# Optimization experiments

Hardware: AMD Instinct MI355X
Metric: run time of the kernel (lower is better)

## Reference

```python
import jax, jax.numpy as jnp
import numpy as np

BETA = 1.0  # inverse temperature (default of retrieve())
EPS = 1e-12  # matches torch F.normalize eps


def _l2_normalize(x):
    # torch.nn.functional.normalize(p=2, dim=-1): x / max(||x||, eps)
    n = jnp.sqrt(jnp.sum(x * x, axis=-1, keepdims=True))
    return x / jnp.maximum(n, EPS)


def setup_inputs() -> dict:
    key = jax.random.key(0)
    kq, kk = jax.random.split(key)
    N, K, D = 65536, 4096, 128
    queries = jax.random.normal(kq, (N, D), dtype=jnp.float32)
    # learnable memory keys, init_std = 0.02
    keys = jax.random.normal(kk, (K, D), dtype=jnp.float32) * 0.02
    return {"queries": queries, "keys": keys}


def reference(queries, keys):
    # normalize_keys=True, normalize_queries=True
    k_n = _l2_normalize(keys)
    q_n = _l2_normalize(queries)
    # values are TIED to the raw keys parameter (get_values returns self.keys,
    # un-normalized) — only the score-side keys are normalized.
    values = keys
    scores = BETA * jnp.einsum('nd,kd->nk', q_n, k_n)  # [N, K]
    attention = jax.nn.softmax(scores, axis=-1)
    retrieved = jnp.einsum('nk,kd->nd', attention, values)  # [N, D]
    return retrieved
```

## Files before the change

### kernel.cpp

```cpp
#include <hip/hip_runtime.h>
#include <hip/hip_bf16.h>
#include <stdint.h>


typedef __attribute__((ext_vector_type(8))) short bf16x8;
typedef __attribute__((ext_vector_type(16))) float f32x16;

#define MFMA32(a, b, c) __builtin_amdgcn_mfma_f32_32x32x16_bf16(a, b, c, 0, 0, 0)

__device__ __forceinline__ unsigned pkbf(float lo, float hi) {
  union { __hip_bfloat162 h2; unsigned u; } v;
  v.h2 = __float22bfloat162_rn(float2{lo, hi});
  return v.u;
}

__global__ __launch_bounds__(256) void prep_k(const float* __restrict__ k,
                                              char* __restrict__ knf,
                                              char* __restrict__ vtf, int K) {
  __shared__ float sRaw[64 * 132];
  __shared__ float sScale[64];
  const int tid = threadIdx.x;
  const int kbase = blockIdx.x * 64;
  {
    const int key_loc = tid >> 2, dq = tid & 3;
    const float4* src = (const float4*)(k + (size_t)(kbase + key_loc) * 128 + dq * 32);
    float4 f[8];
    float ss = 0.f;
#pragma unroll
    for (int i = 0; i < 8; ++i) {
      f[i] = src[i];
      ss += f[i].x * f[i].x + f[i].y * f[i].y + f[i].z * f[i].z + f[i].w * f[i].w;
    }
    ss += __shfl_xor(ss, 1);
    ss += __shfl_xor(ss, 2);
    float4* dst = (float4*)(sRaw + key_loc * 132 + dq * 32);
#pragma unroll
    for (int i = 0; i < 8; ++i) dst[i] = f[i];
    if (dq == 0) sScale[key_loc] = ss > 0.f ? rsqrtf(ss) : 0.f;
  }
  __syncthreads();

#pragma unroll
  for (int r = 0; r < 4; ++r) {
    const int c = r * 256 + tid;
    const int t_loc = c >> 9, ds = (c >> 6) & 7, l = c & 63;
    const int h5 = l >> 5, c32 = l & 31;
    const int key_loc = t_loc * 32 + c32;
    const float sc = sScale[key_loc];
    const float* p = sRaw + key_loc * 132 + ds * 16 + h5 * 8;
    uint4 w;
    w.x = pkbf(p[0] * sc, p[1] * sc);
    w.y = pkbf(p[2] * sc, p[3] * sc);
    w.z = pkbf(p[4] * sc, p[5] * sc);
    w.w = pkbf(p[6] * sc, p[7] * sc);
    *(uint4*)(knf + ((size_t)blockIdx.x * 1024 + c) * 16) = w;
  }
#pragma unroll
  for (int r = 0; r < 4; ++r) {
    const int c = r * 256 + tid;
    const int s = c >> 8, db2 = (c >> 6) & 3, l = c & 63;
    const int h5 = l >> 5, c32 = l & 31;
    const int d = db2 * 32 + c32;
    const int kb = (s >> 1) * 32 + (s & 1) * 8 + h5 * 4;
    float f[8];
#pragma unroll
    for (int j = 0; j < 8; ++j)
      f[j] = sRaw[(kb + (j & 3) + (j >> 2) * 16) * 132 + d];
    uint4 w;
    w.x = pkbf(f[0], f[1]);
    w.y = pkbf(f[2], f[3]);
    w.z = pkbf(f[4], f[5]);
    w.w = pkbf(f[6], f[7]);
    *(uint4*)(vtf + ((size_t)blockIdx.x * 1024 + c) * 16) = w;
  }
}

__global__ __launch_bounds__(256) void attn_main(
    const float* __restrict__ q, const char* __restrict__ knf,
    const char* __restrict__ vtf, float* __restrict__ out, int K) {
  __shared__ __align__(16) char sE[16384];
  const int tid = threadIdx.x;
  const int wave = tid >> 6, lane = tid & 63;
  const int h5 = lane >> 5, c32 = lane & 31;
  const int qrow0 = blockIdx.x * 128 + wave * 32;

  bf16x8 qf[8];
  {
    const float* qr = q + (size_t)(qrow0 + c32) * 128;
    float f[64];
    float ss = 0.f;
#pragma unroll
    for (int ds = 0; ds < 8; ++ds) {
      const float4 a = *(const float4*)(qr + ds * 16 + h5 * 8);
      const float4 b = *(const float4*)(qr + ds * 16 + h5 * 8 + 4);
      f[ds * 8 + 0] = a.x; f[ds * 8 + 1] = a.y; f[ds * 8 + 2] = a.z; f[ds * 8 + 3] = a.w;
      f[ds * 8 + 4] = b.x; f[ds * 8 + 5] = b.y; f[ds * 8 + 6] = b.z; f[ds * 8 + 7] = b.w;
    }
#pragma unroll
    for (int i = 0; i < 64; ++i) ss += f[i] * f[i];
    ss += __shfl_xor(ss, 32);
    const float sc = (ss > 0.f ? rsqrtf(ss) : 0.f) * 1.44269504f;
#pragma unroll
    for (int ds = 0; ds < 8; ++ds) {
      union { unsigned u[4]; bf16x8 v; } t;
#pragma unroll
      for (int p = 0; p < 4; ++p)
        t.u[p] = pkbf(f[ds * 8 + 2 * p] * sc, f[ds * 8 + 2 * p + 1] * sc);
      qf[ds] = t.v;
    }
  }

  f32x16 acc[4];
#pragma unroll
  for (int db2 = 0; db2 < 4; ++db2)
#pragma unroll
    for (int r = 0; r < 16; ++r) acc[db2][r] = 0.f;
  float den = 0.f;
  f32x16 Zf;
#pragma unroll
  for (int r = 0; r < 16; ++r) Zf[r] = 0.f;

  const int nIter = K >> 5;

  auto body = [&](int it, bf16x8 (&kfC)[8], bf16x8 (&kfN)[8]) {
    const int itn = (it + 1 < nIter) ? it + 1 : it;
#pragma unroll
    for (int ds = 0; ds < 8; ++ds)
      kfN[ds] = *(const bf16x8*)(knf + (size_t)itn * 8192 + ds * 1024 + lane * 16);
    bf16x8 vf[8];
#pragma unroll
    for (int j = 0; j < 8; ++j)
      vf[j] = *(const bf16x8*)(vtf + (size_t)it * 8192 + j * 1024 + lane * 16);
    f32x16 S;
#pragma unroll
    for (int ds = 0; ds < 8; ++ds)
      S = MFMA32(kfC[ds], qf[ds], (ds == 0) ? Zf : S);
#pragma unroll
    for (int w = 0; w < 2; ++w) {
      float e[8];
#pragma unroll
      for (int j = 0; j < 8; ++j) {
        const int rr = w * 4 + (j & 3) + (j >> 2) * 8;
        e[j] = __builtin_amdgcn_exp2f(S[rr]);
      }
      den += ((e[0] + e[1]) + (e[2] + e[3])) + ((e[4] + e[5]) + (e[6] + e[7]));
      union { unsigned u[4]; bf16x8 v; } pf;
#pragma unroll
      for (int j2 = 0; j2 < 4; ++j2) pf.u[j2] = pkbf(e[2 * j2], e[2 * j2 + 1]);
#pragma unroll
      for (int db2 = 0; db2 < 4; ++db2)
        acc[db2] = MFMA32(vf[w * 4 + db2], pf.v, acc[db2]);
    }
  };

  bf16x8 kfA[8], kfB[8];
#pragma unroll
  for (int ds = 0; ds < 8; ++ds)
    kfA[ds] = *(const bf16x8*)(knf + ds * 1024 + lane * 16);
  for (int it = 0; it < nIter; it += 2) {
    body(it, kfA, kfB);
    body(it + 1, kfB, kfA);
  }

  den += __shfl_xor(den, 32);
  const float rd = 1.0f / den;

  float* wls = (float*)(sE + wave * 4096);
#pragma unroll
  for (int db2 = 0; db2 < 4; ++db2) {
#pragma unroll
    for (int qd = 0; qd < 4; ++qd) {
      float4 v;
      v.x = acc[db2][qd * 4 + 0] * rd;
      v.y = acc[db2][qd * 4 + 1] * rd;
      v.z = acc[db2][qd * 4 + 2] * rd;
      v.w = acc[db2][qd * 4 + 3] * rd;
      *(float4*)(wls + c32 * 32 + (((h5 + 2 * qd) ^ (c32 & 7)) << 2)) = v;
    }
#pragma unroll
    for (int p = 0; p < 4; ++p) {
      const int ql = p * 8 + (lane >> 3);
      const int x = lane & 7;
      const float4 v = *(const float4*)(wls + ql * 32 + ((x ^ (ql & 7)) << 2));
      *(float4*)(out + (size_t)(qrow0 + ql) * 128 + db2 * 32 + x * 4) = v;
    }
  }
}

extern "C" void kernel_launch(void* const* d_in, const int* in_sizes, int n_in,
                              void* d_out, int out_size, void* d_ws, size_t ws_size,
                              hipStream_t stream) {
  const float* q = (const float*)d_in[0];
  const float* k = (const float*)d_in[1];
  const int N = in_sizes[0] / 128;
  const int K = in_sizes[1] / 128;
  char* ws = (char*)d_ws;
  char* knf = ws;
  char* vtf = ws + (size_t)K * 256;
  float* out = (float*)d_out;

  prep_k<<<dim3(K / 64), dim3(256), 0, stream>>>(k, knf, vtf, K);
  attn_main<<<dim3(N / 128), dim3(256), 0, stream>>>(q, knf, vtf, out, K);
}
```

Before: 225.3 us.

## Split value dimension across grid and process two query tiles per wave

Result: slower. 285.4 us (+26.7%).

```diff
diff --git a/kernel.cpp b/kernel.cpp
--- a/kernel.cpp
+++ b/kernel.cpp
@@ -75,18 +75,20 @@
   }
 }
 
-__global__ __launch_bounds__(256) void attn_main(
+__global__ __launch_bounds__(256, 2) void attn_main(
     const float* __restrict__ q, const char* __restrict__ knf,
     const char* __restrict__ vtf, float* __restrict__ out, int K) {
   __shared__ __align__(16) char sE[16384];
   const int tid = threadIdx.x;
   const int wave = tid >> 6, lane = tid & 63;
   const int h5 = lane >> 5, c32 = lane & 31;
-  const int qrow0 = blockIdx.x * 128 + wave * 32;
-
-  bf16x8 qf[8];
-  {
-    const float* qr = q + (size_t)(qrow0 + c32) * 128;
+  const int split = blockIdx.y;
+  const int qrow0 = blockIdx.x * 256 + wave * 64;
+
+  bf16x8 qf[2][8];
+#pragma unroll
+  for (int qt = 0; qt < 2; ++qt) {
+    const float* qr = q + (size_t)(qrow0 + qt * 32 + c32) * 128;
     float f[64];
     float ss = 0.f;
 #pragma unroll
@@ -106,85 +108,101 @@
 #pragma unroll
       for (int p = 0; p < 4; ++p)
         t.u[p] = pkbf(f[ds * 8 + 2 * p] * sc, f[ds * 8 + 2 * p + 1] * sc);
-      qf[ds] = t.v;
-    }
-  }
-
-  f32x16 acc[4];
-#pragma unroll
-  for (int db2 = 0; db2 < 4; ++db2)
-#pragma unroll
-    for (int r = 0; r < 16; ++r) acc[db2][r] = 0.f;
-  float den = 0.f;
+      qf[qt][ds] = t.v;
+    }
+  }
+
+  f32x16 acc[2][2];
+#pragma unroll
+  for (int dt = 0; dt < 2; ++dt)
+#pragma unroll
+    for (int qt = 0; qt < 2; ++qt)
+#pragma unroll
+      for (int r = 0; r < 16; ++r) acc[dt][qt][r] = 0.f;
+  float den[2] = {0.f, 0.f};
   f32x16 Zf;
 #pragma unroll
   for (int r = 0; r < 16; ++r) Zf[r] = 0.f;
 
   const int nIter = K >> 5;
-
-  auto body = [&](int it, bf16x8 (&kfC)[8], bf16x8 (&kfN)[8]) {
-    const int itn = (it + 1 < nIter) ? it + 1 : it;
+  const char* vsp = vtf + split * 2048;
+
+#pragma unroll 2
+  for (int it = 0; it < nIter; ++it) {
+    bf16x8 kf[8];
 #pragma unroll
     for (int ds = 0; ds < 8; ++ds)
-      kfN[ds] = *(const bf16x8*)(knf + (size_t)itn * 8192 + ds * 1024 + lane * 16);
-    bf16x8 vf[8];
-#pragma unroll
-    for (int j = 0; j < 8; ++j)
-      vf[j] = *(const bf16x8*)(vtf + (size_t)it * 8192 + j * 1024 + lane * 16);
-    f32x16 S;
-#pragma unroll
-    for (int ds = 0; ds < 8; ++ds)
-      S = MFMA32(kfC[ds], qf[ds], (ds == 0) ? Zf : S);
+      kf[ds] = *(const bf16x8*)(knf + (size_t)it * 8192 + ds * 1024 + lane * 16);
+    bf16x8 vf[2][2];
+#pragma unroll
+    for (int w = 0; w < 2; ++w)
+#pragma unroll
+      for (int dt = 0; dt < 2; ++dt)
+        vf[w][dt] = *(const bf16x8*)(vsp + (size_t)(it * 2 + w) * 4096 +
+                                     dt * 1024 + lane * 16);
+
+    f32x16 S[2];
+#pragma unroll
+    for (int qt = 0; qt < 2; ++qt) {
+      f32x16 s;
+#pragma unroll
+      for (int ds = 0; ds < 8; ++ds)
+        s = MFMA32(kf[ds], qf[qt][ds], (ds == 0) ? Zf : s);
+      S[qt] = s;
+    }
+
 #pragma unroll
     for (int w = 0; w < 2; ++w) {
-      float e[8];
-#pragma unroll
-      for (int j = 0; j < 8; ++j) {
-        const int rr = w * 4 + (j & 3) + (j >> 2) * 8;
-        e[j] = __builtin_amdgcn_exp2f(S[rr]);
+#pragma unroll
+      for (int qt = 0; qt < 2; ++qt) {
+        float e[8];
+#pragma unroll
+        for (int j = 0; j < 8; ++j) {
+          const int rr = w * 4 + (j & 3) + (j >> 2) * 8;
+          e[j] = __builtin_amdgcn_exp2f(S[qt][rr]);
+        }
+        den[qt] += ((e[0] + e[1]) + (e[2] + e[3])) + ((e[4] + e[5]) + (e[6] + e[7]));
+        union { unsigned u[4]; bf16x8 v; } pf;
+#pragma unroll
+        for (int j2 = 0; j2 < 4; ++j2) pf.u[j2] = pkbf(e[2 * j2], e[2 * j2 + 1]);
+#pragma unroll
+        for (int dt = 0; dt < 2; ++dt)
+          acc[dt][qt] = MFMA32(vf[w][dt], pf.v, acc[dt][qt]);
       }
-      den += ((e[0] + e[1]) + (e[2] + e[3])) + ((e[4] + e[5]) + (e[6] + e[7]));
-      union { unsigned u[4]; bf16x8 v; } pf;
-#pragma unroll
-      for (int j2 = 0; j2 < 4; ++j2) pf.u[j2] = pkbf(e[2 * j2], e[2 * j2 + 1]);
-#pragma unroll
-      for (int db2 = 0; db2 < 4; ++db2)
-        acc[db2] = MFMA32(vf[w * 4 + db2], pf.v, acc[db2]);
-    }
-  };
-
-  bf16x8 kfA[8], kfB[8];
-#pragma unroll
-  for (int ds = 0; ds < 8; ++ds)
-    kfA[ds] = *(const bf16x8*)(knf + ds * 1024 + lane * 16);
-  for (int it = 0; it < nIter; it += 2) {
-    body(it, kfA, kfB);
-    body(it + 1, kfB, kfA);
-  }
-
-  den += __shfl_xor(den, 32);
-  const float rd = 1.0f / den;
+    }
+  }
+
+  float rd[2];
+#pragma unroll
+  for (int qt = 0; qt < 2; ++qt) {
+    float d = den[qt];
+    d += __shfl_xor(d, 32);
+    rd[qt] = 1.0f / d;
+  }
 
   float* wls = (float*)(sE + wave * 4096);
 #pragma unroll
-  for (int db2 = 0; db2 < 4; ++db2) {
-#pragma unroll
-    for (int qd = 0; qd < 4; ++qd) {
-      float4 v;
-      v.x = acc[db2][qd * 4 + 0] * rd;
-      v.y = acc[db2][qd * 4 + 1] * rd;
-      v.z = acc[db2][qd * 4 + 2] * rd;
-      v.w = acc[db2][qd * 4 + 3] * rd;
-      *(float4*)(wls + c32 * 32 + (((h5 + 2 * qd) ^ (c32 & 7)) << 2)) = v;
-    }
-#pragma unroll
-    for (int p = 0; p < 4; ++p) {
-      const int ql = p * 8 + (lane >> 3);
-      const int x = lane & 7;
-      const float4 v = *(const float4*)(wls + ql * 32 + ((x ^ (ql & 7)) << 2));
-      *(float4*)(out + (size_t)(qrow0 + ql) * 128 + db2 * 32 + x * 4) = v;
-    }
-  }
+  for (int dt = 0; dt < 2; ++dt)
+#pragma unroll
+    for (int qt = 0; qt < 2; ++qt) {
+#pragma unroll
+      for (int qd = 0; qd < 4; ++qd) {
+        float4 v;
+        v.x = acc[dt][qt][qd * 4 + 0] * rd[qt];
+        v.y = acc[dt][qt][qd * 4 + 1] * rd[qt];
+        v.z = acc[dt][qt][qd * 4 + 2] * rd[qt];
+        v.w = acc[dt][qt][qd * 4 + 3] * rd[qt];
+        *(float4*)(wls + c32 * 32 + (((h5 + 2 * qd) ^ (c32 & 7)) << 2)) = v;
+      }
+#pragma unroll
+      for (int p = 0; p < 4; ++p) {
+        const int ql = p * 8 + (lane >> 3);
+        const int x = lane & 7;
+        const float4 v = *(const float4*)(wls + ql * 32 + ((x ^ (ql & 7)) << 2));
+        *(float4*)(out + (size_t)(qrow0 + qt * 32 + ql) * 128 + split * 64 +
+                   dt * 32 + x * 4) = v;
+      }
+    }
 }
 
 extern "C" void kernel_launch(void* const* d_in, const int* in_sizes, int n_in,
@@ -200,5 +218,5 @@
   float* out = (float*)d_out;
 
   prep_k<<<dim3(K / 64), dim3(256), 0, stream>>>(k, knf, vtf, K);
-  attn_main<<<dim3(N / 128), dim3(256), 0, stream>>>(q, knf, vtf, out, K);
-}
+  attn_main<<<dim3(N / 256, 2), dim3(256), 0, stream>>>(q, knf, vtf, out, K);
+}
```

## Split QK MFMA chain and alternate software-pipeline schedules across blocks

Applied to the files above, without the earlier changes.

Result: slower. 272.5 us (+21.0%).

```diff
diff --git a/kernel.cpp b/kernel.cpp
--- a/kernel.cpp
+++ b/kernel.cpp
@@ -122,26 +122,31 @@
 
   const int nIter = K >> 5;
 
-  auto body = [&](int it, bf16x8 (&kfC)[8], bf16x8 (&kfN)[8]) {
-    const int itn = (it + 1 < nIter) ? it + 1 : it;
+  auto loadK = [&](int it, bf16x8 (&kf)[8]) {
+    if (it >= nIter) it = nIter - 1;
 #pragma unroll
     for (int ds = 0; ds < 8; ++ds)
-      kfN[ds] = *(const bf16x8*)(knf + (size_t)itn * 8192 + ds * 1024 + lane * 16);
-    bf16x8 vf[8];
+      kf[ds] = *(const bf16x8*)(knf + (size_t)it * 8192 + ds * 1024 + lane * 16);
+  };
+  auto loadV = [&](int it, bf16x8 (&vf)[8]) {
 #pragma unroll
     for (int j = 0; j < 8; ++j)
       vf[j] = *(const bf16x8*)(vtf + (size_t)it * 8192 + j * 1024 + lane * 16);
-    f32x16 S;
-#pragma unroll
-    for (int ds = 0; ds < 8; ++ds)
-      S = MFMA32(kfC[ds], qf[ds], (ds == 0) ? Zf : S);
+  };
+  auto computeS = [&](const bf16x8 (&kf)[8], f32x16& s0, f32x16& s1) {
+#pragma unroll
+    for (int ds = 0; ds < 4; ++ds) s0 = MFMA32(kf[ds], qf[ds], ds ? s0 : Zf);
+#pragma unroll
+    for (int ds = 4; ds < 8; ++ds) s1 = MFMA32(kf[ds], qf[ds], ds > 4 ? s1 : Zf);
+  };
+  auto expPV = [&](const bf16x8 (&vf)[8], const f32x16& s0, const f32x16& s1) {
 #pragma unroll
     for (int w = 0; w < 2; ++w) {
       float e[8];
 #pragma unroll
       for (int j = 0; j < 8; ++j) {
         const int rr = w * 4 + (j & 3) + (j >> 2) * 8;
-        e[j] = __builtin_amdgcn_exp2f(S[rr]);
+        e[j] = __builtin_amdgcn_exp2f(s0[rr] + s1[rr]);
       }
       den += ((e[0] + e[1]) + (e[2] + e[3])) + ((e[4] + e[5]) + (e[6] + e[7]));
       union { unsigned u[4]; bf16x8 v; } pf;
@@ -153,13 +158,33 @@
     }
   };
 
-  bf16x8 kfA[8], kfB[8];
-#pragma unroll
-  for (int ds = 0; ds < 8; ++ds)
-    kfA[ds] = *(const bf16x8*)(knf + ds * 1024 + lane * 16);
-  for (int it = 0; it < nIter; it += 2) {
-    body(it, kfA, kfB);
-    body(it + 1, kfB, kfA);
+  const int rot = (blockIdx.x ^ (blockIdx.x >> 3) ^ (blockIdx.x >> 8)) & 1;
+
+  bf16x8 kfA[8], kfB[8], vfS[8];
+  f32x16 s0, s1;
+  if (!rot) {
+    loadK(0, kfA);
+    for (int it = 0; it < nIter; it += 2) {
+      loadK(it + 1, kfB);
+      computeS(kfA, s0, s1);
+      loadV(it, vfS);
+      expPV(vfS, s0, s1);
+      loadK(it + 2, kfA);
+      computeS(kfB, s0, s1);
+      loadV(it + 1, vfS);
+      expPV(vfS, s0, s1);
+    }
+  } else {
+    loadK(0, kfA);
+    computeS(kfA, s0, s1);
+    for (int it = 0; it < nIter - 1; ++it) {
+      loadK(it + 1, kfA);
+      loadV(it, vfS);
+      expPV(vfS, s0, s1);
+      computeS(kfA, s0, s1);
+    }
+    loadV(nIter - 1, vfS);
+    expPV(vfS, s0, s1);
   }
 
   den += __shfl_xor(den, 32);
```
